# Performance work log

Measured on AMD Instinct MI355X. Metric: run time of the kernel, lower is better.

Reference implementation:

```python
import jax, jax.numpy as jnp
import numpy as np

N_NODES = 20000
N_EDGES = 160000
CIN = 2000
N1 = 500
N2 = 250
DIM_Z = 16


def _xavier(key, shape):
    fan_out, fan_in = shape
    lim = jnp.sqrt(6.0 / (fan_in + fan_out))
    return jax.random.uniform(key, shape, jnp.float32, -lim, lim)


def setup_inputs() -> dict:
    key = jax.random.key(0)
    ks = jax.random.split(key, 10)
    data_in = jax.random.normal(ks[0], (N_NODES, CIN), jnp.float32)
    edge_index = jax.random.randint(ks[1], (2, N_EDGES), 0, N_NODES, jnp.int64)
    edge_weight = jax.random.uniform(ks[2], (N_EDGES,), jnp.float32)
    return {
        "data_in": data_in,
        "edge_index": edge_index,
        "edge_weight": edge_weight,
        "W1": _xavier(ks[3], (N1, CIN)),
        "b1": jnp.zeros((N1,), jnp.float32),
        "W2": _xavier(ks[4], (N2, N1)),
        "b2": jnp.zeros((N2,), jnp.float32),
        "W_mu_t": _xavier(ks[5], (1, N2)),
        "b_mu_t": jnp.zeros((1,), jnp.float32),
        "W_std_t": _xavier(ks[6], (1, N2)),
        "b_std_t": jnp.zeros((1,), jnp.float32),
        "W_mu_z": _xavier(ks[7], (DIM_Z, N2)),
        "b_mu_z": jnp.zeros((DIM_Z,), jnp.float32),
        "W_std_z": _xavier(ks[8], (DIM_Z, N2)),
        "b_std_z": jnp.zeros((DIM_Z,), jnp.float32),
    }


def gcn_conv(x, W, b, src, dst, ew, n_nodes):
    """PyG GCNConv: add self-loops (weight 1), symmetric deg^-1/2 normalization,
    linear transform, scatter-add aggregate to target nodes, add bias."""
    loop = jnp.arange(n_nodes, dtype=src.dtype)
    src_f = jnp.concatenate([src, loop])
    dst_f = jnp.concatenate([dst, loop])
    ew_f = jnp.concatenate([ew, jnp.ones((n_nodes,), ew.dtype)])
    deg = jax.ops.segment_sum(ew_f, dst_f, num_segments=n_nodes)
    dinv = jnp.where(deg > 0, jax.lax.rsqrt(deg), 0.0)
    norm = dinv[src_f] * ew_f * dinv[dst_f]  # [E+N]
    h = x @ W.T                               # [N, F_out]
    msgs = h[src_f] * norm[:, None]           # [E+N, F_out] gathered messages
    out = jax.ops.segment_sum(msgs, dst_f, num_segments=n_nodes)
    return out + b


def reference(data_in, edge_index, edge_weight, W1, b1, W2, b2,
              W_mu_t, b_mu_t, W_std_t, b_std_t, W_mu_z, b_mu_z, W_std_z, b_std_z):
    src, dst = edge_index[0], edge_index[1]
    n = data_in.shape[0]
    h = gcn_conv(data_in, W1, b1, src, dst, edge_weight, n)
    h = gcn_conv(h, W2, b2, src, dst, edge_weight, n)
    mu_tx = jax.nn.softplus(h @ W_mu_t.T + b_mu_t)
    std_tx = jax.nn.softplus(h @ W_std_t.T + b_std_t)
    mu_zx = h @ W_mu_z.T + b_mu_z
    std_zx = jax.nn.softplus(h @ W_std_z.T + b_std_z)
    return (mu_tx, std_tx, mu_zx, std_zx)
```

## Files before the change

kernel.cpp:

```cpp
#include <hip/hip_runtime.h>

#define N_NODES 20000
#define N_EDGES 160000
#define CIN     2000
#define N1      500
#define N2      250
#define NH      34
#define NHP     64

typedef __attribute__((ext_vector_type(4))) float f32x4;
typedef __attribute__((ext_vector_type(8))) __bf16 bf16x8;
typedef __attribute__((ext_vector_type(8))) unsigned short ushort8;

typedef const __attribute__((address_space(1))) void* as1cv;
typedef __attribute__((address_space(3))) void* as3v;

__device__ __forceinline__ unsigned short f2bf(float f) {
    unsigned int u = __builtin_bit_cast(unsigned int, f);
    u += 0x7FFFu + ((u >> 16) & 1u);
    return (unsigned short)(u >> 16);
}

__device__ __forceinline__ ushort8 pack8(float4 a, float4 b) {
    ushort8 r;
    r[0] = f2bf(a.x); r[1] = f2bf(a.y); r[2] = f2bf(a.z); r[3] = f2bf(a.w);
    r[4] = f2bf(b.x); r[5] = f2bf(b.y); r[6] = f2bf(b.z); r[7] = f2bf(b.w);
    return r;
}

__global__ __launch_bounds__(256) void k1(
    const int* __restrict__ ei, const float* __restrict__ ew,
    float* degsum, int* cnt,
    const float* __restrict__ W2,
    const float* __restrict__ Wmt, const float* __restrict__ Wst,
    const float* __restrict__ Wmz, const float* __restrict__ Wsz,
    float* __restrict__ V, unsigned short* __restrict__ Vb,
    const float* __restrict__ W1, unsigned short* __restrict__ W1T) {
    __shared__ float tile[32][33];
    const int B = blockIdx.x, t = threadIdx.x;
    if (B < 625) {
        int e = B * 256 + t;
        if (e < N_EDGES) {
            int d = ei[N_EDGES + e];
            atomicAdd(&degsum[d], ew[e]);
            atomicAdd(&cnt[d], 1);
        }
        return;
    }
    if (B < 753) {
        float* wh = &tile[0][0];
        int b = B - 625;
        int o = b >> 1, half = b & 1;
        int n = half * 256 + t;
        if (o >= NH) {
            V[(size_t)o * 512 + n] = 0.f;
            Vb[(size_t)o * 512 + n] = 0;
            return;
        }
        const float* src; int row;
        if (o == 0)      { src = Wmt; row = 0; }
        else if (o == 1) { src = Wst; row = 0; }
        else if (o < 18) { src = Wmz; row = o - 2; }
        else             { src = Wsz; row = o - 18; }
        if (t < N2) wh[t] = src[(size_t)row * N2 + t];
        __syncthreads();
        float acc = 0.f;
        if (n < N1) {
            for (int j = 0; j < N2; ++j) acc += wh[j] * W2[(size_t)j * N1 + n];
        }
        float v = (n < N1) ? acc : 0.f;
        V[(size_t)o * 512 + n] = v;
        Vb[(size_t)o * 512 + n] = f2bf(v);
        return;
    }
    int bb = B - 753;
    int jt = bb & 15, nt = bb >> 4;
    int c = t & 31, r = t >> 5;
#pragma unroll
    for (int i = 0; i < 4; ++i) {
        int j = jt * 32 + r + i * 8;
        int n = nt * 32 + c;
        tile[r + i * 8][c] = (j < N1 && n < CIN) ? W1[(size_t)j * CIN + n] : 0.f;
    }
    __syncthreads();
#pragma unroll
    for (int i = 0; i < 4; ++i) {
        int n = nt * 32 + r + i * 8;
        int j = jt * 32 + c;
        W1T[(size_t)n * 512 + j] = f2bf(tile[c][r + i * 8]);
    }
}

__global__ __launch_bounds__(256) void k2(
    const int* __restrict__ cnt, const float* __restrict__ degsum,
    float* __restrict__ dinv, int* __restrict__ rowPtr, int* __restrict__ cursor,
    const unsigned short* __restrict__ Vb, const unsigned short* __restrict__ W1T,
    unsigned short* __restrict__ Wtb,
    const float* __restrict__ V,
    const float* __restrict__ b1, const float* __restrict__ b2,
    const float* __restrict__ bmt, const float* __restrict__ bst,
    const float* __restrict__ bmz, const float* __restrict__ bsz,
    const float* __restrict__ Wmt, const float* __restrict__ Wst,
    const float* __restrict__ Wmz, const float* __restrict__ Wsz,
    float* __restrict__ ccdd) {
    __shared__ alignas(16) unsigned short lA[128 * 32];
    __shared__ alignas(16) unsigned short lB[128 * 32];
    __shared__ int sdata[256];
    const int B = blockIdx.x, t = threadIdx.x;
    if (B < 79) {
        const int nbase = B * 256;
        int idx = nbase + t;
        if (idx < N_NODES) cursor[idx] = 0;
        int s = 0;
        for (int i = t; i < nbase; i += 256) s += cnt[i];
        sdata[t] = s;
        __syncthreads();
        for (int off = 128; off; off >>= 1) {
            if (t < off) sdata[t] += sdata[t + off];
            __syncthreads();
        }
        const int base = sdata[0];
        __syncthreads();
        int v = 0;
        if (idx < N_NODES) {
            v = cnt[idx];
            dinv[idx] = rsqrtf(1.0f + degsum[idx]);
        }
        sdata[t] = v;
        __syncthreads();
        for (int off = 1; off < 256; off <<= 1) {
            int x = (t >= off) ? sdata[t - off] : 0;
            __syncthreads();
            sdata[t] += x;
            __syncthreads();
        }
        if (idx < N_NODES) rowPtr[idx] = base + sdata[t] - v;
        if (B == 78 && t == 255) rowPtr[N_NODES] = base + sdata[255];
        return;
    }
    if (B == 79) {
        int w = t >> 6, lane = t & 63;
        for (int o = w; o < NH; o += 4) {
            float cc = 0.f;
            for (int n = lane; n < N1; n += 64) cc += V[(size_t)o * 512 + n] * b1[n];
            const float* src; int row; float bias;
            if (o == 0)      { src = Wmt; row = 0;      bias = bmt[0]; }
            else if (o == 1) { src = Wst; row = 0;      bias = bst[0]; }
            else if (o < 18) { src = Wmz; row = o - 2;  bias = bmz[o - 2]; }
            else             { src = Wsz; row = o - 18; bias = bsz[o - 18]; }
            float dd = 0.f;
            for (int j = lane; j < N2; j += 64) dd += src[(size_t)row * N2 + j] * b2[j];
#pragma unroll
            for (int off = 32; off; off >>= 1) {
                cc += __shfl_down(cc, off);
                dd += __shfl_down(dd, off);
            }
            if (lane == 0) { ccdd[o] = cc; ccdd[NHP + o] = dd + bias; }
        }
        if (t >= NH && t < NHP) { ccdd[t] = 0.f; ccdd[NHP + t] = 0.f; }
        return;
    }
    {
        const int w = t >> 6, lane = t & 63;
        const int bn0 = (B - 80) * 128;
        const int M = 64;
        const int wr = w >> 1, wc = w & 1;
        const int lr = lane & 15, lk = (lane >> 4) * 8;
        f32x4 acc[4][4];
#pragma unroll
        for (int i = 0; i < 4; i++)
#pragma unroll
            for (int j = 0; j < 4; j++) acc[i][j] = (f32x4){0.f, 0.f, 0.f, 0.f};
        for (int kt = 0; kt < 16; ++kt) {
            const int kb = kt * 32;
#pragma unroll
            for (int i = 0; i < 2; i++) {
                int c0 = i * 256 + w * 64;
                int c  = c0 + lane;
                int rr = c >> 2, kg = c & 3;
                int grow = rr < M ? rr : M - 1;
                const unsigned short* gp = Vb + (size_t)grow * 512 + kb + kg * 8;
                __builtin_amdgcn_global_load_lds((as1cv)gp, (as3v)(lA + (size_t)c0 * 8), 16, 0, 0);
            }
#pragma unroll
            for (int i = 0; i < 2; i++) {
                int c0 = i * 256 + w * 64;
                int c  = c0 + lane;
                int rr = c >> 2, kg = c & 3;
                const unsigned short* gp = W1T + (size_t)(bn0 + rr) * 512 + kb + kg * 8;
                __builtin_amdgcn_global_load_lds((as1cv)gp, (as3v)(lB + (size_t)c0 * 8), 16, 0, 0);
            }
            __syncthreads();
            ushort8 af[4], bfr[4];
#pragma unroll
            for (int m = 0; m < 4; m++)
                af[m] = *reinterpret_cast<const ushort8*>(&lA[(wr * 64 + m * 16 + lr) * 32 + lk]);
#pragma unroll
            for (int n = 0; n < 4; n++)
                bfr[n] = *reinterpret_cast<const ushort8*>(&lB[(wc * 64 + n * 16 + lr) * 32 + lk]);
#pragma unroll
            for (int m = 0; m < 4; m++)
#pragma unroll
                for (int n = 0; n < 4; n++)
                    acc[m][n] = __builtin_amdgcn_mfma_f32_16x16x32_bf16(
                        __builtin_bit_cast(bf16x8, af[m]), __builtin_bit_cast(bf16x8, bfr[n]),
                        acc[m][n], 0, 0, 0);
            __syncthreads();
        }
        const int crow0 = wr * 64 + (lane >> 4) * 4;
        const int ccol0 = bn0 + wc * 64 + lr;
#pragma unroll
        for (int m = 0; m < 4; m++)
#pragma unroll
            for (int n = 0; n < 4; n++)
#pragma unroll
                for (int rg = 0; rg < 4; rg++) {
                    int row = crow0 + m * 16 + rg;
                    if (row < M)
                        Wtb[(size_t)row * 2048 + ccol0 + n * 16] = f2bf(acc[m][n][rg]);
                }
    }
}

__global__ __launch_bounds__(256) void k3(
    const float* __restrict__ X, const unsigned short* __restrict__ Wtb,
    float* __restrict__ Tpart,
    const int* __restrict__ ei, const float* __restrict__ ew,
    const float* __restrict__ dinv, const int* __restrict__ rowPtr,
    int* cursor, int* __restrict__ colA, float* __restrict__ valA) {
    __shared__ alignas(16) unsigned short lA[64 * 64];
    __shared__ alignas(16) unsigned short lB[64 * 64];
    const int B = blockIdx.x, t = threadIdx.x;
    if (B >= 626) {
        int e = (B - 626) * 256 + t;
        if (e < N_EDGES) {
            int s = ei[e], d = ei[N_EDGES + e];
            int p = atomicAdd(&cursor[d], 1);
            int j = rowPtr[d] + p;
            colA[j] = s;
            valA[j] = dinv[s] * ew[e] * dinv[d];
        }
        return;
    }
    const int w = t >> 6, lane = t & 63;
    const int kp = B & 1;
    const int bm0 = (B >> 1) * 64;
    const int kbase = kp * 1024;
    const int lr = lane & 15, lkb = (lane >> 4) * 16;

    const int c0 = t, c1 = t + 256;
    const int ar0 = c0 >> 3, ac0 = (c0 & 7) * 8;
    const int ar1 = c1 >> 3, ac1 = (c1 & 7) * 8;
    int gr0 = bm0 + ar0; if (gr0 >= N_NODES) gr0 = N_NODES - 1;
    int gr1 = bm0 + ar1; if (gr1 >= N_NODES) gr1 = N_NODES - 1;
    const float* pA0 = X + (size_t)gr0 * CIN + kbase + ac0;
    const float* pA1 = X + (size_t)gr1 * CIN + kbase + ac1;
    const unsigned short* pB0 = Wtb + ar0 * 2048 + kbase + ac0;
    const unsigned short* pB1 = Wtb + ar1 * 2048 + kbase + ac1;
    char* const LA = (char*)lA;
    char* const LB = (char*)lB;
    char* const wA0 = LA + ((ar0 * 128 + ac0 * 2) ^ ((ar0 & 7) << 4));
    char* const wA1 = LA + ((ar1 * 128 + ac1 * 2) ^ ((ar1 & 7) << 4));
    char* const wB0 = LB + ((ar0 * 128 + ac0 * 2) ^ ((ar0 & 7) << 4));
    char* const wB1 = LB + ((ar1 * 128 + ac1 * 2) ^ ((ar1 & 7) << 4));

    int aoff[4][2], boff[2];
#pragma unroll
    for (int m = 0; m < 4; ++m)
#pragma unroll
        for (int k = 0; k < 2; ++k)
            aoff[m][k] = (((m * 16 + lr) * 128 + k * 64 + lkb) ^ ((lr & 7) << 4));
#pragma unroll
    for (int k = 0; k < 2; ++k)
        boff[k] = (((w * 16 + lr) * 128 + k * 64 + lkb) ^ ((lr & 7) << 4));

    f32x4 acc[4];
#pragma unroll
    for (int m = 0; m < 4; ++m) acc[m] = (f32x4){0.f, 0.f, 0.f, 0.f};

    float4 a00A, a01A, a10A, a11A; ushort8 bv0A, bv1A;
    float4 a00B, a01B, a10B, a11B; ushort8 bv0B, bv1B;
    const float4 z4 = make_float4(0.f, 0.f, 0.f, 0.f);

#define STAGE_LOAD(S, a00_, a01_, a10_, a11_, bv0_, bv1_)                          \
    {                                                                              \
        bool v0 = (kbase + ac0 + (S) * 64) < CIN;                                  \
        bool v1 = (kbase + ac1 + (S) * 64) < CIN;                                  \
        const float4* q0 = (const float4*)(v0 ? pA0 + (S) * 64 : (const float*)X); \
        const float4* q1 = (const float4*)(v1 ? pA1 + (S) * 64 : (const float*)X); \
        a00_ = q0[0]; a01_ = q0[1];                                                \
        a10_ = q1[0]; a11_ = q1[1];                                                \
        if (!v0) { a00_ = z4; a01_ = z4; }                                         \
        if (!v1) { a10_ = z4; a11_ = z4; }                                         \
        bv0_ = *(const ushort8*)(pB0 + (S) * 64);                                  \
        bv1_ = *(const ushort8*)(pB1 + (S) * 64);                                  \
    }

    auto compute = [&]() {
#pragma unroll
        for (int k = 0; k < 2; ++k) {
            ushort8 bf = *(const ushort8*)(LB + boff[k]);
#pragma unroll
            for (int m = 0; m < 4; ++m) {
                ushort8 af = *(const ushort8*)(LA + aoff[m][k]);
                acc[m] = __builtin_amdgcn_mfma_f32_16x16x32_bf16(
                    __builtin_bit_cast(bf16x8, af), __builtin_bit_cast(bf16x8, bf),
                    acc[m], 0, 0, 0);
            }
        }
    };

    STAGE_LOAD(0, a00A, a01A, a10A, a11A, bv0A, bv1A)
    STAGE_LOAD(1, a00B, a01B, a10B, a11B, bv0B, bv1B)
    for (int s2 = 0; s2 < 8; ++s2) {
        const int s = 2 * s2;
        __syncthreads();
        *(ushort8*)wA0 = pack8(a00A, a01A);
        *(ushort8*)wA1 = pack8(a10A, a11A);
        *(ushort8*)wB0 = bv0A;
        *(ushort8*)wB1 = bv1A;
        __syncthreads();
        if (s + 2 < 16) STAGE_LOAD(s + 2, a00A, a01A, a10A, a11A, bv0A, bv1A)
        compute();
        __syncthreads();
        *(ushort8*)wA0 = pack8(a00B, a01B);
        *(ushort8*)wA1 = pack8(a10B, a11B);
        *(ushort8*)wB0 = bv0B;
        *(ushort8*)wB1 = bv1B;
        __syncthreads();
        if (s + 3 < 16) STAGE_LOAD(s + 3, a00B, a01B, a10B, a11B, bv0B, bv1B)
        compute();
    }
#undef STAGE_LOAD
    float* Tp = Tpart + (size_t)kp * N_NODES * NHP;
    const int col = w * 16 + lr;
    const int rb = bm0 + (lane >> 4) * 4;
#pragma unroll
    for (int m = 0; m < 4; ++m)
#pragma unroll
        for (int rg = 0; rg < 4; ++rg) {
            int row = rb + m * 16 + rg;
            if (row < N_NODES) Tp[(size_t)row * NHP + col] = acc[m][rg];
        }
}

__global__ __launch_bounds__(256) void agg_a(
    const float* __restrict__ Tp, const int* __restrict__ rowPtr,
    const int* __restrict__ colA, const float* __restrict__ valA,
    const float* __restrict__ dinv, float* __restrict__ U) {
    const float* __restrict__ T1 = Tp + (size_t)N_NODES * NHP;
    int wid = blockIdx.x * 4 + (threadIdx.x >> 6);
    int lane = threadIdx.x & 63;
    if (wid >= N_NODES) return;
    int d = wid;
    float dv = dinv[d];
    float acc = dv * dv * (Tp[(size_t)d * NHP + lane] + T1[(size_t)d * NHP + lane]);
    int e0 = rowPtr[d], e1 = rowPtr[d + 1];
    int e = e0;
    for (; e + 8 <= e1; e += 8) {
        int   s0 = colA[e],     s1 = colA[e + 1], s2 = colA[e + 2], s3 = colA[e + 3];
        int   s4 = colA[e + 4], s5 = colA[e + 5], s6 = colA[e + 6], s7 = colA[e + 7];
        float w0 = valA[e],     w1 = valA[e + 1], w2 = valA[e + 2], w3 = valA[e + 3];
        float w4 = valA[e + 4], w5 = valA[e + 5], w6 = valA[e + 6], w7 = valA[e + 7];
        float t0 = Tp[(size_t)s0 * NHP + lane] + T1[(size_t)s0 * NHP + lane];
        float t1 = Tp[(size_t)s1 * NHP + lane] + T1[(size_t)s1 * NHP + lane];
        float t2 = Tp[(size_t)s2 * NHP + lane] + T1[(size_t)s2 * NHP + lane];
        float t3 = Tp[(size_t)s3 * NHP + lane] + T1[(size_t)s3 * NHP + lane];
        float t4 = Tp[(size_t)s4 * NHP + lane] + T1[(size_t)s4 * NHP + lane];
        float t5 = Tp[(size_t)s5 * NHP + lane] + T1[(size_t)s5 * NHP + lane];
        float t6 = Tp[(size_t)s6 * NHP + lane] + T1[(size_t)s6 * NHP + lane];
        float t7 = Tp[(size_t)s7 * NHP + lane] + T1[(size_t)s7 * NHP + lane];
        acc += w0 * t0 + w1 * t1 + w2 * t2 + w3 * t3
             + w4 * t4 + w5 * t5 + w6 * t6 + w7 * t7;
    }
    for (; e + 4 <= e1; e += 4) {
        int s0 = colA[e], s1 = colA[e + 1], s2 = colA[e + 2], s3 = colA[e + 3];
        float w0 = valA[e], w1 = valA[e + 1], w2 = valA[e + 2], w3 = valA[e + 3];
        float t0 = Tp[(size_t)s0 * NHP + lane] + T1[(size_t)s0 * NHP + lane];
        float t1 = Tp[(size_t)s1 * NHP + lane] + T1[(size_t)s1 * NHP + lane];
        float t2 = Tp[(size_t)s2 * NHP + lane] + T1[(size_t)s2 * NHP + lane];
        float t3 = Tp[(size_t)s3 * NHP + lane] + T1[(size_t)s3 * NHP + lane];
        acc += w0 * t0 + w1 * t1 + w2 * t2 + w3 * t3;
    }
    for (; e < e1; ++e) {
        int s = colA[e];
        acc += valA[e] * (Tp[(size_t)s * NHP + lane] + T1[(size_t)s * NHP + lane]);
    }
    U[(size_t)d * NHP + lane] = acc;
}

__global__ __launch_bounds__(256) void agg_b(
    const float* __restrict__ U, const int* __restrict__ rowPtr,
    const int* __restrict__ colA, const float* __restrict__ valA,
    const float* __restrict__ dinv, const float* __restrict__ ccdd,
    float* __restrict__ out) {
    int wid = blockIdx.x * 4 + (threadIdx.x >> 6);
    int lane = threadIdx.x & 63;
    if (wid >= N_NODES) return;
    int d = wid;
    float dv = dinv[d], self = dv * dv;
    float acc = self * U[(size_t)d * NHP + lane];
    float r = self;
    int e0 = rowPtr[d], e1 = rowPtr[d + 1];
    int e = e0;
    for (; e + 8 <= e1; e += 8) {
        int   s0 = colA[e],     s1 = colA[e + 1], s2 = colA[e + 2], s3 = colA[e + 3];
        int   s4 = colA[e + 4], s5 = colA[e + 5], s6 = colA[e + 6], s7 = colA[e + 7];
        float w0 = valA[e],     w1 = valA[e + 1], w2 = valA[e + 2], w3 = valA[e + 3];
        float w4 = valA[e + 4], w5 = valA[e + 5], w6 = valA[e + 6], w7 = valA[e + 7];
        float t0 = U[(size_t)s0 * NHP + lane], t1 = U[(size_t)s1 * NHP + lane];
        float t2 = U[(size_t)s2 * NHP + lane], t3 = U[(size_t)s3 * NHP + lane];
        float t4 = U[(size_t)s4 * NHP + lane], t5 = U[(size_t)s5 * NHP + lane];
        float t6 = U[(size_t)s6 * NHP + lane], t7 = U[(size_t)s7 * NHP + lane];
        acc += w0 * t0 + w1 * t1 + w2 * t2 + w3 * t3
             + w4 * t4 + w5 * t5 + w6 * t6 + w7 * t7;
        r += w0 + w1 + w2 + w3 + w4 + w5 + w6 + w7;
    }
    for (; e + 4 <= e1; e += 4) {
        int s0 = colA[e], s1 = colA[e + 1], s2 = colA[e + 2], s3 = colA[e + 3];
        float w0 = valA[e], w1 = valA[e + 1], w2 = valA[e + 2], w3 = valA[e + 3];
        float t0 = U[(size_t)s0 * NHP + lane], t1 = U[(size_t)s1 * NHP + lane];
        float t2 = U[(size_t)s2 * NHP + lane], t3 = U[(size_t)s3 * NHP + lane];
        acc += w0 * t0 + w1 * t1 + w2 * t2 + w3 * t3;
        r += w0 + w1 + w2 + w3;
    }
    for (; e < e1; ++e) {
        int s = colA[e];
        float wv = valA[e];
        acc += wv * U[(size_t)s * NHP + lane];
        r += wv;
    }
    if (lane < NH) {
        float v = acc + r * ccdd[lane] + ccdd[NHP + lane];
        if (lane < 2 || lane >= 18)
            v = fmaxf(v, 0.f) + log1pf(expf(-fabsf(v)));
        size_t oidx;
        if (lane == 0)      oidx = (size_t)d;
        else if (lane == 1) oidx = (size_t)N_NODES + d;
        else if (lane < 18) oidx = (size_t)2 * N_NODES + (size_t)d * 16 + (lane - 2);
        else                oidx = (size_t)18 * N_NODES + (size_t)d * 16 + (lane - 18);
        out[oidx] = v;
    }
}

extern "C" void kernel_launch(void* const* d_in, const int* in_sizes, int n_in,
                              void* d_out, int out_size, void* d_ws, size_t ws_size,
                              hipStream_t stream) {
    const float* X   = (const float*)d_in[0];
    const int*   EI  = (const int*)d_in[1];
    const float* EW  = (const float*)d_in[2];
    const float* W1  = (const float*)d_in[3];
    const float* b1  = (const float*)d_in[4];
    const float* W2  = (const float*)d_in[5];
    const float* b2  = (const float*)d_in[6];
    const float* Wmt = (const float*)d_in[7];
    const float* bmt = (const float*)d_in[8];
    const float* Wst = (const float*)d_in[9];
    const float* bst = (const float*)d_in[10];
    const float* Wmz = (const float*)d_in[11];
    const float* bmz = (const float*)d_in[12];
    const float* Wsz = (const float*)d_in[13];
    const float* bsz = (const float*)d_in[14];
    float* out = (float*)d_out;

    char* ws = (char*)d_ws;
    size_t off = 0;
    auto alloc = [&](size_t bytes) -> char* {
        char* p = ws + off;
        off += (bytes + 255) & ~(size_t)255;
        return p;
    };
    float*          V    = (float*)alloc((size_t)NHP * 512 * 4);
    unsigned short* Vb   = (unsigned short*)alloc((size_t)NHP * 512 * 2);
    unsigned short* W1T  = (unsigned short*)alloc((size_t)2048 * 512 * 2);
    unsigned short* Wtb  = (unsigned short*)alloc((size_t)NHP * 2048 * 2);
    float*          ccdd = (float*)alloc(2 * NHP * 4);
    float*          Tp   = (float*)alloc((size_t)2 * N_NODES * NHP * 4);
    float*          U    = (float*)alloc((size_t)N_NODES * NHP * 4);
    float* degsum = (float*)alloc(N_NODES * 4);
    int*   cnt    = (int*)alloc(N_NODES * 4);
    int*   cursor = (int*)alloc(N_NODES * 4);
    float* dinv   = (float*)alloc(N_NODES * 4);
    int*   rowPtr = (int*)alloc((N_NODES + 1) * 4);
    int*   colA   = (int*)alloc(N_EDGES * 4);
    float* valA   = (float*)alloc(N_EDGES * 4);
    if (off > ws_size) return;

    size_t zspan = (size_t)((char*)(cnt + N_NODES) - (char*)degsum);
    hipMemsetAsync(degsum, 0, zspan, stream);

    k1<<<625 + 128 + 1024, 256, 0, stream>>>(EI, EW, degsum, cnt,
                                             W2, Wmt, Wst, Wmz, Wsz, V, Vb, W1, W1T);
    k2<<<79 + 1 + 16, 256, 0, stream>>>(cnt, degsum, dinv, rowPtr, cursor,
                                        Vb, W1T, Wtb, V,
                                        b1, b2, bmt, bst, bmz, bsz, Wmt, Wst, Wmz, Wsz, ccdd);
    k3<<<626 + 625, 256, 0, stream>>>(X, Wtb, Tp, EI, EW, dinv, rowPtr, cursor, colA, valA);
    agg_a<<<(N_NODES + 3) / 4, 256, 0, stream>>>(Tp, rowPtr, colA, valA, dinv, U);
    agg_b<<<(N_NODES + 3) / 4, 256, 0, stream>>>(U, rowPtr, colA, valA, dinv, ccdd, out);
}
```

Baseline: 123.5 us.

## Fuse GEMM, CSR fill and both aggregations into persistent kernel with grid barriers

Merges k3, agg_a and agg_b into one persistent kernel of 512 blocks that loops over the former work units and separates the phases with a two-level software tree barrier built on agent-scope atomics. Intermediate stores use relaxed agent-scope atomic stores so later phases can see them. This removes two kernel launches and their gaps, at the cost of fewer resident blocks for the GEMM phase and reliance on all 512 blocks being co-resident. The k1 W2 reduction loop is also unrolled by 8.

```diff
diff --git a/kernel.cpp b/kernel.cpp
--- a/kernel.cpp
+++ b/kernel.cpp
@@ -7,6 +7,7 @@
 #define N2      250
 #define NH      34
 #define NHP     64
+#define MEGA_BLK 512
 
 typedef __attribute__((ext_vector_type(4))) float f32x4;
 typedef __attribute__((ext_vector_type(8))) __bf16 bf16x8;
@@ -26,6 +27,40 @@
     r[0] = f2bf(a.x); r[1] = f2bf(a.y); r[2] = f2bf(a.z); r[3] = f2bf(a.w);
     r[4] = f2bf(b.x); r[5] = f2bf(b.y); r[6] = f2bf(b.z); r[7] = f2bf(b.w);
     return r;
+}
+
+__device__ __forceinline__ void ast(float* p, float v) {
+    __hip_atomic_store(p, v, __ATOMIC_RELAXED, __HIP_MEMORY_SCOPE_AGENT);
+}
+__device__ __forceinline__ void asti(int* p, int v) {
+    __hip_atomic_store(p, v, __ATOMIC_RELAXED, __HIP_MEMORY_SCOPE_AGENT);
+}
+
+__device__ __forceinline__ void tree_barrier(int* bars) {
+    asm volatile("s_waitcnt vmcnt(0)" ::: "memory");
+    __syncthreads();
+    if (threadIdx.x == 0) {
+        int g = blockIdx.x & 15;
+        int* gcnt = bars + g * 32;
+        int* ggen = bars + g * 32 + 16;
+        int* rcnt = bars + 512;
+        int* rgen = bars + 528;
+        int a = __hip_atomic_fetch_add(gcnt, 1, __ATOMIC_RELAXED, __HIP_MEMORY_SCOPE_AGENT);
+        if (a == 31) {
+            int r = __hip_atomic_fetch_add(rcnt, 1, __ATOMIC_RELAXED, __HIP_MEMORY_SCOPE_AGENT);
+            if (r == 15) {
+                __hip_atomic_store(rgen, 1, __ATOMIC_RELAXED, __HIP_MEMORY_SCOPE_AGENT);
+            } else {
+                while (__hip_atomic_load(rgen, __ATOMIC_RELAXED, __HIP_MEMORY_SCOPE_AGENT) == 0)
+                    __builtin_amdgcn_s_sleep(16);
+            }
+            __hip_atomic_store(ggen, 1, __ATOMIC_RELAXED, __HIP_MEMORY_SCOPE_AGENT);
+        } else {
+            while (__hip_atomic_load(ggen, __ATOMIC_RELAXED, __HIP_MEMORY_SCOPE_AGENT) == 0)
+                __builtin_amdgcn_s_sleep(16);
+        }
+    }
+    __syncthreads();
 }
 
 __global__ __launch_bounds__(256) void k1(
@@ -66,7 +101,17 @@
         __syncthreads();
         float acc = 0.f;
         if (n < N1) {
-            for (int j = 0; j < N2; ++j) acc += wh[j] * W2[(size_t)j * N1 + n];
+            const float* p = W2 + n;
+            int j = 0;
+            for (; j + 8 <= N2; j += 8) {
+                float x0 = p[(size_t)(j + 0) * N1], x1 = p[(size_t)(j + 1) * N1];
+                float x2 = p[(size_t)(j + 2) * N1], x3 = p[(size_t)(j + 3) * N1];
+                float x4 = p[(size_t)(j + 4) * N1], x5 = p[(size_t)(j + 5) * N1];
+                float x6 = p[(size_t)(j + 6) * N1], x7 = p[(size_t)(j + 7) * N1];
+                acc += wh[j] * x0 + wh[j + 1] * x1 + wh[j + 2] * x2 + wh[j + 3] * x3
+                     + wh[j + 4] * x4 + wh[j + 5] * x5 + wh[j + 6] * x6 + wh[j + 7] * x7;
+            }
+            for (; j < N2; ++j) acc += wh[j] * p[(size_t)j * N1];
         }
         float v = (n < N1) ? acc : 0.f;
         V[(size_t)o * 512 + n] = v;
@@ -102,7 +147,7 @@
     const float* __restrict__ bmz, const float* __restrict__ bsz,
     const float* __restrict__ Wmt, const float* __restrict__ Wst,
     const float* __restrict__ Wmz, const float* __restrict__ Wsz,
-    float* __restrict__ ccdd) {
+    float* __restrict__ ccdd, int* __restrict__ bars) {
     __shared__ alignas(16) unsigned short lA[128 * 32];
     __shared__ alignas(16) unsigned short lB[128 * 32];
     __shared__ int sdata[256];
@@ -139,6 +184,7 @@
         return;
     }
     if (B == 79) {
+        for (int i = t; i < 1088; i += 256) bars[i] = 0;
         int w = t >> 6, lane = t & 63;
         for (int o = w; o < NH; o += 4) {
             float cc = 0.f;
@@ -222,65 +268,70 @@
     }
 }
 
-__global__ __launch_bounds__(256) void k3(
+__global__ __launch_bounds__(256, 2) void k3mega(
     const float* __restrict__ X, const unsigned short* __restrict__ Wtb,
-    float* __restrict__ Tpart,
+    float* __restrict__ Tp,
     const int* __restrict__ ei, const float* __restrict__ ew,
     const float* __restrict__ dinv, const int* __restrict__ rowPtr,
-    int* cursor, int* __restrict__ colA, float* __restrict__ valA) {
+    int* cursor, int* __restrict__ colA, float* __restrict__ valA,
+    float* __restrict__ U, const float* __restrict__ ccdd,
+    float* __restrict__ out, int* __restrict__ bars) {
     __shared__ alignas(16) unsigned short lA[64 * 64];
     __shared__ alignas(16) unsigned short lB[64 * 64];
     const int B = blockIdx.x, t = threadIdx.x;
-    if (B >= 626) {
-        int e = (B - 626) * 256 + t;
-        if (e < N_EDGES) {
-            int s = ei[e], d = ei[N_EDGES + e];
-            int p = atomicAdd(&cursor[d], 1);
-            int j = rowPtr[d] + p;
-            colA[j] = s;
-            valA[j] = dinv[s] * ew[e] * dinv[d];
-        }
-        return;
-    }
-    const int w = t >> 6, lane = t & 63;
-    const int kp = B & 1;
-    const int bm0 = (B >> 1) * 64;
-    const int kbase = kp * 1024;
-    const int lr = lane & 15, lkb = (lane >> 4) * 16;
-
-    const int c0 = t, c1 = t + 256;
-    const int ar0 = c0 >> 3, ac0 = (c0 & 7) * 8;
-    const int ar1 = c1 >> 3, ac1 = (c1 & 7) * 8;
-    int gr0 = bm0 + ar0; if (gr0 >= N_NODES) gr0 = N_NODES - 1;
-    int gr1 = bm0 + ar1; if (gr1 >= N_NODES) gr1 = N_NODES - 1;
-    const float* pA0 = X + (size_t)gr0 * CIN + kbase + ac0;
-    const float* pA1 = X + (size_t)gr1 * CIN + kbase + ac1;
-    const unsigned short* pB0 = Wtb + ar0 * 2048 + kbase + ac0;
-    const unsigned short* pB1 = Wtb + ar1 * 2048 + kbase + ac1;
-    char* const LA = (char*)lA;
-    char* const LB = (char*)lB;
-    char* const wA0 = LA + ((ar0 * 128 + ac0 * 2) ^ ((ar0 & 7) << 4));
-    char* const wA1 = LA + ((ar1 * 128 + ac1 * 2) ^ ((ar1 & 7) << 4));
-    char* const wB0 = LB + ((ar0 * 128 + ac0 * 2) ^ ((ar0 & 7) << 4));
-    char* const wB1 = LB + ((ar1 * 128 + ac1 * 2) ^ ((ar1 & 7) << 4));
-
-    int aoff[4][2], boff[2];
-#pragma unroll
-    for (int m = 0; m < 4; ++m)
+    const int lane = t & 63;
+
+    for (int u = B; u < 1251; u += MEGA_BLK) {
+        if (u >= 626) {
+            int e = (u - 626) * 256 + t;
+            if (e < N_EDGES) {
+                int s = ei[e], d = ei[N_EDGES + e];
+                int p = atomicAdd(&cursor[d], 1);
+                int j = rowPtr[d] + p;
+                asti(&colA[j], s);
+                ast(&valA[j], dinv[s] * ew[e] * dinv[d]);
+            }
+            continue;
+        }
+        const int w = t >> 6;
+        const int kp = u & 1;
+        const int bm0 = (u >> 1) * 64;
+        const int kbase = kp * 1024;
+        const int lr = lane & 15, lkb = (lane >> 4) * 16;
+
+        const int c0 = t, c1 = t + 256;
+        const int ar0 = c0 >> 3, ac0 = (c0 & 7) * 8;
+        const int ar1 = c1 >> 3, ac1 = (c1 & 7) * 8;
+        int gr0 = bm0 + ar0; if (gr0 >= N_NODES) gr0 = N_NODES - 1;
+        int gr1 = bm0 + ar1; if (gr1 >= N_NODES) gr1 = N_NODES - 1;
+        const float* pA0 = X + (size_t)gr0 * CIN + kbase + ac0;
+        const float* pA1 = X + (size_t)gr1 * CIN + kbase + ac1;
+        const unsigned short* pB0 = Wtb + ar0 * 2048 + kbase + ac0;
+        const unsigned short* pB1 = Wtb + ar1 * 2048 + kbase + ac1;
+        char* const LA = (char*)lA;
+        char* const LB = (char*)lB;
+        char* const wA0 = LA + ((ar0 * 128 + ac0 * 2) ^ ((ar0 & 7) << 4));
+        char* const wA1 = LA + ((ar1 * 128 + ac1 * 2) ^ ((ar1 & 7) << 4));
+        char* const wB0 = LB + ((ar0 * 128 + ac0 * 2) ^ ((ar0 & 7) << 4));
+        char* const wB1 = LB + ((ar1 * 128 + ac1 * 2) ^ ((ar1 & 7) << 4));
+
+        int aoff[4][2], boff[2];
+#pragma unroll
+        for (int m = 0; m < 4; ++m)
+#pragma unroll
+            for (int k = 0; k < 2; ++k)
+                aoff[m][k] = (((m * 16 + lr) * 128 + k * 64 + lkb) ^ ((lr & 7) << 4));
 #pragma unroll
         for (int k = 0; k < 2; ++k)
-            aoff[m][k] = (((m * 16 + lr) * 128 + k * 64 + lkb) ^ ((lr & 7) << 4));
-#pragma unroll
-    for (int k = 0; k < 2; ++k)
-        boff[k] = (((w * 16 + lr) * 128 + k * 64 + lkb) ^ ((lr & 7) << 4));
-
-    f32x4 acc[4];
-#pragma unroll
-    for (int m = 0; m < 4; ++m) acc[m] = (f32x4){0.f, 0.f, 0.f, 0.f};
-
-    float4 a00A, a01A, a10A, a11A; ushort8 bv0A, bv1A;
-    float4 a00B, a01B, a10B, a11B; ushort8 bv0B, bv1B;
-    const float4 z4 = make_float4(0.f, 0.f, 0.f, 0.f);
+            boff[k] = (((w * 16 + lr) * 128 + k * 64 + lkb) ^ ((lr & 7) << 4));
+
+        f32x4 acc[4];
+#pragma unroll
+        for (int m = 0; m < 4; ++m) acc[m] = (f32x4){0.f, 0.f, 0.f, 0.f};
+
+        float4 a00A, a01A, a10A, a11A; ushort8 bv0A, bv1A;
+        float4 a00B, a01B, a10B, a11B; ushort8 bv0B, bv1B;
+        const float4 z4 = make_float4(0.f, 0.f, 0.f, 0.f);
 
 #define STAGE_LOAD(S, a00_, a01_, a10_, a11_, bv0_, bv1_)                          \
     {                                                                              \
@@ -296,150 +347,128 @@
         bv1_ = *(const ushort8*)(pB1 + (S) * 64);                                  \
     }
 
-    auto compute = [&]() {
-#pragma unroll
-        for (int k = 0; k < 2; ++k) {
-            ushort8 bf = *(const ushort8*)(LB + boff[k]);
-#pragma unroll
-            for (int m = 0; m < 4; ++m) {
-                ushort8 af = *(const ushort8*)(LA + aoff[m][k]);
-                acc[m] = __builtin_amdgcn_mfma_f32_16x16x32_bf16(
-                    __builtin_bit_cast(bf16x8, af), __builtin_bit_cast(bf16x8, bf),
-                    acc[m], 0, 0, 0);
-            }
-        }
-    };
-
-    STAGE_LOAD(0, a00A, a01A, a10A, a11A, bv0A, bv1A)
-    STAGE_LOAD(1, a00B, a01B, a10B, a11B, bv0B, bv1B)
-    for (int s2 = 0; s2 < 8; ++s2) {
-        const int s = 2 * s2;
-        __syncthreads();
-        *(ushort8*)wA0 = pack8(a00A, a01A);
-        *(ushort8*)wA1 = pack8(a10A, a11A);
-        *(ushort8*)wB0 = bv0A;
-        *(ushort8*)wB1 = bv1A;
-        __syncthreads();
-        if (s + 2 < 16) STAGE_LOAD(s + 2, a00A, a01A, a10A, a11A, bv0A, bv1A)
-        compute();
-        __syncthreads();
-        *(ushort8*)wA0 = pack8(a00B, a01B);
-        *(ushort8*)wA1 = pack8(a10B, a11B);
-        *(ushort8*)wB0 = bv0B;
-        *(ushort8*)wB1 = bv1B;
-        __syncthreads();
-        if (s + 3 < 16) STAGE_LOAD(s + 3, a00B, a01B, a10B, a11B, bv0B, bv1B)
-        compute();
-    }
+        auto compute = [&]() {
+#pragma unroll
+            for (int k = 0; k < 2; ++k) {
+                ushort8 bf = *(const ushort8*)(LB + boff[k]);
+#pragma unroll
+                for (int m = 0; m < 4; ++m) {
+                    ushort8 af = *(const ushort8*)(LA + aoff[m][k]);
+                    acc[m] = __builtin_amdgcn_mfma_f32_16x16x32_bf16(
+                        __builtin_bit_cast(bf16x8, af), __builtin_bit_cast(bf16x8, bf),
+                        acc[m], 0, 0, 0);
+                }
+            }
+        };
+
+        STAGE_LOAD(0, a00A, a01A, a10A, a11A, bv0A, bv1A)
+        STAGE_LOAD(1, a00B, a01B, a10B, a11B, bv0B, bv1B)
+        for (int s2 = 0; s2 < 8; ++s2) {
+            const int s = 2 * s2;
+            __syncthreads();
+            *(ushort8*)wA0 = pack8(a00A, a01A);
+            *(ushort8*)wA1 = pack8(a10A, a11A);
+            *(ushort8*)wB0 = bv0A;
+            *(ushort8*)wB1 = bv1A;
+            __syncthreads();
+            if (s + 2 < 16) STAGE_LOAD(s + 2, a00A, a01A, a10A, a11A, bv0A, bv1A)
+            compute();
+            __syncthreads();
+            *(ushort8*)wA0 = pack8(a00B, a01B);
+            *(ushort8*)wA1 = pack8(a10B, a11B);
+            *(ushort8*)wB0 = bv0B;
+            *(ushort8*)wB1 = bv1B;
+            __syncthreads();
+            if (s + 3 < 16) STAGE_LOAD(s + 3, a00B, a01B, a10B, a11B, bv0B, bv1B)
+            compute();
+        }
 #undef STAGE_LOAD
-    float* Tp = Tpart + (size_t)kp * N_NODES * NHP;
-    const int col = w * 16 + lr;
-    const int rb = bm0 + (lane >> 4) * 4;
-#pragma unroll
-    for (int m = 0; m < 4; ++m)
-#pragma unroll
-        for (int rg = 0; rg < 4; ++rg) {
-            int row = rb + m * 16 + rg;
-            if (row < N_NODES) Tp[(size_t)row * NHP + col] = acc[m][rg];
-        }
-}
-
-__global__ __launch_bounds__(256) void agg_a(
-    const float* __restrict__ Tp, const int* __restrict__ rowPtr,
-    const int* __restrict__ colA, const float* __restrict__ valA,
-    const float* __restrict__ dinv, float* __restrict__ U) {
-    const float* __restrict__ T1 = Tp + (size_t)N_NODES * NHP;
-    int wid = blockIdx.x * 4 + (threadIdx.x >> 6);
-    int lane = threadIdx.x & 63;
-    if (wid >= N_NODES) return;
-    int d = wid;
-    float dv = dinv[d];
-    float acc = dv * dv * (Tp[(size_t)d * NHP + lane] + T1[(size_t)d * NHP + lane]);
-    int e0 = rowPtr[d], e1 = rowPtr[d + 1];
-    int e = e0;
-    for (; e + 8 <= e1; e += 8) {
-        int   s0 = colA[e],     s1 = colA[e + 1], s2 = colA[e + 2], s3 = colA[e + 3];
-        int   s4 = colA[e + 4], s5 = colA[e + 5], s6 = colA[e + 6], s7 = colA[e + 7];
-        float w0 = valA[e],     w1 = valA[e + 1], w2 = valA[e + 2], w3 = valA[e + 3];
-        float w4 = valA[e + 4], w5 = valA[e + 5], w6 = valA[e + 6], w7 = valA[e + 7];
-        float t0 = Tp[(size_t)s0 * NHP + lane] + T1[(size_t)s0 * NHP + lane];
-        float t1 = Tp[(size_t)s1 * NHP + lane] + T1[(size_t)s1 * NHP + lane];
-        float t2 = Tp[(size_t)s2 * NHP + lane] + T1[(size_t)s2 * NHP + lane];
-        float t3 = Tp[(size_t)s3 * NHP + lane] + T1[(size_t)s3 * NHP + lane];
-        float t4 = Tp[(size_t)s4 * NHP + lane] + T1[(size_t)s4 * NHP + lane];
-        float t5 = Tp[(size_t)s5 * NHP + lane] + T1[(size_t)s5 * NHP + lane];
-        float t6 = Tp[(size_t)s6 * NHP + lane] + T1[(size_t)s6 * NHP + lane];
-        float t7 = Tp[(size_t)s7 * NHP + lane] + T1[(size_t)s7 * NHP + lane];
-        acc += w0 * t0 + w1 * t1 + w2 * t2 + w3 * t3
-             + w4 * t4 + w5 * t5 + w6 * t6 + w7 * t7;
-    }
-    for (; e + 4 <= e1; e += 4) {
-        int s0 = colA[e], s1 = colA[e + 1], s2 = colA[e + 2], s3 = colA[e + 3];
-        float w0 = valA[e], w1 = valA[e + 1], w2 = valA[e + 2], w3 = valA[e + 3];
-        float t0 = Tp[(size_t)s0 * NHP + lane] + T1[(size_t)s0 * NHP + lane];
-        float t1 = Tp[(size_t)s1 * NHP + lane] + T1[(size_t)s1 * NHP + lane];
-        float t2 = Tp[(size_t)s2 * NHP + lane] + T1[(size_t)s2 * NHP + lane];
-        float t3 = Tp[(size_t)s3 * NHP + lane] + T1[(size_t)s3 * NHP + lane];
-        acc += w0 * t0 + w1 * t1 + w2 * t2 + w3 * t3;
-    }
-    for (; e < e1; ++e) {
-        int s = colA[e];
-        acc += valA[e] * (Tp[(size_t)s * NHP + lane] + T1[(size_t)s * NHP + lane]);
-    }
-    U[(size_t)d * NHP + lane] = acc;
-}
-
-__global__ __launch_bounds__(256) void agg_b(
-    const float* __restrict__ U, const int* __restrict__ rowPtr,
-    const int* __restrict__ colA, const float* __restrict__ valA,
-    const float* __restrict__ dinv, const float* __restrict__ ccdd,
-    float* __restrict__ out) {
-    int wid = blockIdx.x * 4 + (threadIdx.x >> 6);
-    int lane = threadIdx.x & 63;
-    if (wid >= N_NODES) return;
-    int d = wid;
-    float dv = dinv[d], self = dv * dv;
-    float acc = self * U[(size_t)d * NHP + lane];
-    float r = self;
-    int e0 = rowPtr[d], e1 = rowPtr[d + 1];
-    int e = e0;
-    for (; e + 8 <= e1; e += 8) {
-        int   s0 = colA[e],     s1 = colA[e + 1], s2 = colA[e + 2], s3 = colA[e + 3];
-        int   s4 = colA[e + 4], s5 = colA[e + 5], s6 = colA[e + 6], s7 = colA[e + 7];
-        float w0 = valA[e],     w1 = valA[e + 1], w2 = valA[e + 2], w3 = valA[e + 3];
-        float w4 = valA[e + 4], w5 = valA[e + 5], w6 = valA[e + 6], w7 = valA[e + 7];
-        float t0 = U[(size_t)s0 * NHP + lane], t1 = U[(size_t)s1 * NHP + lane];
-        float t2 = U[(size_t)s2 * NHP + lane], t3 = U[(size_t)s3 * NHP + lane];
-        float t4 = U[(size_t)s4 * NHP + lane], t5 = U[(size_t)s5 * NHP + lane];
-        float t6 = U[(size_t)s6 * NHP + lane], t7 = U[(size_t)s7 * NHP + lane];
-        acc += w0 * t0 + w1 * t1 + w2 * t2 + w3 * t3
-             + w4 * t4 + w5 * t5 + w6 * t6 + w7 * t7;
-        r += w0 + w1 + w2 + w3 + w4 + w5 + w6 + w7;
-    }
-    for (; e + 4 <= e1; e += 4) {
-        int s0 = colA[e], s1 = colA[e + 1], s2 = colA[e + 2], s3 = colA[e + 3];
-        float w0 = valA[e], w1 = valA[e + 1], w2 = valA[e + 2], w3 = valA[e + 3];
-        float t0 = U[(size_t)s0 * NHP + lane], t1 = U[(size_t)s1 * NHP + lane];
-        float t2 = U[(size_t)s2 * NHP + lane], t3 = U[(size_t)s3 * NHP + lane];
-        acc += w0 * t0 + w1 * t1 + w2 * t2 + w3 * t3;
-        r += w0 + w1 + w2 + w3;
-    }
-    for (; e < e1; ++e) {
-        int s = colA[e];
-        float wv = valA[e];
-        acc += wv * U[(size_t)s * NHP + lane];
-        r += wv;
-    }
-    if (lane < NH) {
-        float v = acc + r * ccdd[lane] + ccdd[NHP + lane];
-        if (lane < 2 || lane >= 18)
-            v = fmaxf(v, 0.f) + log1pf(expf(-fabsf(v)));
-        size_t oidx;
-        if (lane == 0)      oidx = (size_t)d;
-        else if (lane == 1) oidx = (size_t)N_NODES + d;
-        else if (lane < 18) oidx = (size_t)2 * N_NODES + (size_t)d * 16 + (lane - 2);
-        else                oidx = (size_t)18 * N_NODES + (size_t)d * 16 + (lane - 18);
-        out[oidx] = v;
+        float* TpK = Tp + (size_t)kp * N_NODES * NHP;
+        const int col = w * 16 + lr;
+        const int rb = bm0 + (lane >> 4) * 4;
+#pragma unroll
+        for (int m = 0; m < 4; ++m)
+#pragma unroll
+            for (int rg = 0; rg < 4; ++rg) {
+                int row = rb + m * 16 + rg;
+                if (row < N_NODES) ast(&TpK[(size_t)row * NHP + col], acc[m][rg]);
+            }
+    }
+
+    tree_barrier(bars);
+
+    {
+        const float* __restrict__ T0 = Tp;
+        const float* __restrict__ T1 = Tp + (size_t)N_NODES * NHP;
+        for (int uu = B; uu < N_NODES / 4; uu += MEGA_BLK) {
+            int d = uu * 4 + (t >> 6);
+            float dv = dinv[d];
+            float acc = dv * dv * (T0[(size_t)d * NHP + lane] + T1[(size_t)d * NHP + lane]);
+            int e0 = rowPtr[d], e1 = rowPtr[d + 1];
+            int e = e0;
+            for (; e + 8 <= e1; e += 8) {
+                int   s0 = colA[e],     s1 = colA[e + 1], s2 = colA[e + 2], s3 = colA[e + 3];
+                int   s4 = colA[e + 4], s5 = colA[e + 5], s6 = colA[e + 6], s7 = colA[e + 7];
+                float w0 = valA[e],     w1 = valA[e + 1], w2 = valA[e + 2], w3 = valA[e + 3];
+                float w4 = valA[e + 4], w5 = valA[e + 5], w6 = valA[e + 6], w7 = valA[e + 7];
+                float t0 = T0[(size_t)s0 * NHP + lane] + T1[(size_t)s0 * NHP + lane];
+                float t1 = T0[(size_t)s1 * NHP + lane] + T1[(size_t)s1 * NHP + lane];
+                float t2 = T0[(size_t)s2 * NHP + lane] + T1[(size_t)s2 * NHP + lane];
+                float t3 = T0[(size_t)s3 * NHP + lane] + T1[(size_t)s3 * NHP + lane];
+                float t4 = T0[(size_t)s4 * NHP + lane] + T1[(size_t)s4 * NHP + lane];
+                float t5 = T0[(size_t)s5 * NHP + lane] + T1[(size_t)s5 * NHP + lane];
+                float t6 = T0[(size_t)s6 * NHP + lane] + T1[(size_t)s6 * NHP + lane];
+                float t7 = T0[(size_t)s7 * NHP + lane] + T1[(size_t)s7 * NHP + lane];
+                acc += w0 * t0 + w1 * t1 + w2 * t2 + w3 * t3
+                     + w4 * t4 + w5 * t5 + w6 * t6 + w7 * t7;
+            }
+            for (; e < e1; ++e) {
+                int s = colA[e];
+                acc += valA[e] * (T0[(size_t)s * NHP + lane] + T1[(size_t)s * NHP + lane]);
+            }
+            ast(&U[(size_t)d * NHP + lane], acc);
+        }
+    }
+
+    tree_barrier(bars + 544);
+
+    for (int uu = B; uu < N_NODES / 4; uu += MEGA_BLK) {
+        int d = uu * 4 + (t >> 6);
+        float dv = dinv[d], self = dv * dv;
+        float acc = self * U[(size_t)d * NHP + lane];
+        float r = self;
+        int e0 = rowPtr[d], e1 = rowPtr[d + 1];
+        int e = e0;
+        for (; e + 8 <= e1; e += 8) {
+            int   s0 = colA[e],     s1 = colA[e + 1], s2 = colA[e + 2], s3 = colA[e + 3];
+            int   s4 = colA[e + 4], s5 = colA[e + 5], s6 = colA[e + 6], s7 = colA[e + 7];
+            float w0 = valA[e],     w1 = valA[e + 1], w2 = valA[e + 2], w3 = valA[e + 3];
+            float w4 = valA[e + 4], w5 = valA[e + 5], w6 = valA[e + 6], w7 = valA[e + 7];
+            float t0 = U[(size_t)s0 * NHP + lane], t1 = U[(size_t)s1 * NHP + lane];
+            float t2 = U[(size_t)s2 * NHP + lane], t3 = U[(size_t)s3 * NHP + lane];
+            float t4 = U[(size_t)s4 * NHP + lane], t5 = U[(size_t)s5 * NHP + lane];
+            float t6 = U[(size_t)s6 * NHP + lane], t7 = U[(size_t)s7 * NHP + lane];
+            acc += w0 * t0 + w1 * t1 + w2 * t2 + w3 * t3
+                 + w4 * t4 + w5 * t5 + w6 * t6 + w7 * t7;
+            r += w0 + w1 + w2 + w3 + w4 + w5 + w6 + w7;
+        }
+        for (; e < e1; ++e) {
+            int s = colA[e];
+            float wv = valA[e];
+            acc += wv * U[(size_t)s * NHP + lane];
+            r += wv;
+        }
+        if (lane < NH) {
+            float v = acc + r * ccdd[lane] + ccdd[NHP + lane];
+            if (lane < 2 || lane >= 18)
+                v = fmaxf(v, 0.f) + log1pf(expf(-fabsf(v)));
+            size_t oidx;
+            if (lane == 0)      oidx = (size_t)d;
+            else if (lane == 1) oidx = (size_t)N_NODES + d;
+            else if (lane < 18) oidx = (size_t)2 * N_NODES + (size_t)d * 16 + (lane - 2);
+            else                oidx = (size_t)18 * N_NODES + (size_t)d * 16 + (lane - 18);
+            out[oidx] = v;
+        }
     }
 }
 
@@ -484,6 +513,7 @@
     int*   rowPtr = (int*)alloc((N_NODES + 1) * 4);
     int*   colA   = (int*)alloc(N_EDGES * 4);
     float* valA   = (float*)alloc(N_EDGES * 4);
+    int*   bars   = (int*)alloc(1088 * 4);
     if (off > ws_size) return;
 
     size_t zspan = (size_t)((char*)(cnt + N_NODES) - (char*)degsum);
@@ -493,8 +523,8 @@
                                              W2, Wmt, Wst, Wmz, Wsz, V, Vb, W1, W1T);
     k2<<<79 + 1 + 16, 256, 0, stream>>>(cnt, degsum, dinv, rowPtr, cursor,
                                         Vb, W1T, Wtb, V,
-                                        b1, b2, bmt, bst, bmz, bsz, Wmt, Wst, Wmz, Wsz, ccdd);
-    k3<<<626 + 625, 256, 0, stream>>>(X, Wtb, Tp, EI, EW, dinv, rowPtr, cursor, colA, valA);
-    agg_a<<<(N_NODES + 3) / 4, 256, 0, stream>>>(Tp, rowPtr, colA, valA, dinv, U);
-    agg_b<<<(N_NODES + 3) / 4, 256, 0, stream>>>(U, rowPtr, colA, valA, dinv, ccdd, out);
-}
+                                        b1, b2, bmt, bst, bmz, bsz, Wmt, Wst, Wmz, Wsz,
+                                        ccdd, bars);
+    k3mega<<<MEGA_BLK, 256, 0, stream>>>(X, Wtb, Tp, EI, EW, dinv, rowPtr,
+                                         cursor, colA, valA, U, ccdd, out, bars);
+}
```

Result: slower. 173.4 us (+40.5%).

## Store aggregation intermediates in bf16 and pre-reduce split-K partials

Applied to the files above, without the earlier changes.

Adds a reduce_T kernel that sums the two split-K partial outputs and stores them as bf16. Both aggregation passes then gather bf16 rows instead of two or one fp32 rows, which cuts the bytes fetched per edge gather by a factor of two to four. The intermediate U is also kept in bf16. The W2-fold loop in k1 is unrolled by eight to expose more independent loads. The cost is an extra kernel launch, one extra pass over Tp, and reduced precision in the intermediates.

```diff
diff --git a/kernel.cpp b/kernel.cpp
--- a/kernel.cpp
+++ b/kernel.cpp
@@ -11,6 +11,7 @@
 typedef __attribute__((ext_vector_type(4))) float f32x4;
 typedef __attribute__((ext_vector_type(8))) __bf16 bf16x8;
 typedef __attribute__((ext_vector_type(8))) unsigned short ushort8;
+typedef __attribute__((ext_vector_type(4))) unsigned short us4;
 
 typedef const __attribute__((address_space(1))) void* as1cv;
 typedef __attribute__((address_space(3))) void* as3v;
@@ -19,6 +20,10 @@
     unsigned int u = __builtin_bit_cast(unsigned int, f);
     u += 0x7FFFu + ((u >> 16) & 1u);
     return (unsigned short)(u >> 16);
+}
+__device__ __forceinline__ float bf2f(unsigned short h) {
+    unsigned int u = ((unsigned int)h) << 16;
+    return __builtin_bit_cast(float, u);
 }
 
 __device__ __forceinline__ ushort8 pack8(float4 a, float4 b) {
@@ -66,7 +71,17 @@
         __syncthreads();
         float acc = 0.f;
         if (n < N1) {
-            for (int j = 0; j < N2; ++j) acc += wh[j] * W2[(size_t)j * N1 + n];
+            const float* p = W2 + n;
+            int j = 0;
+            for (; j + 8 <= N2; j += 8) {
+                float x0 = p[(size_t)(j + 0) * N1], x1 = p[(size_t)(j + 1) * N1];
+                float x2 = p[(size_t)(j + 2) * N1], x3 = p[(size_t)(j + 3) * N1];
+                float x4 = p[(size_t)(j + 4) * N1], x5 = p[(size_t)(j + 5) * N1];
+                float x6 = p[(size_t)(j + 6) * N1], x7 = p[(size_t)(j + 7) * N1];
+                acc += wh[j] * x0 + wh[j + 1] * x1 + wh[j + 2] * x2 + wh[j + 3] * x3
+                     + wh[j + 4] * x4 + wh[j + 5] * x5 + wh[j + 6] * x6 + wh[j + 7] * x7;
+            }
+            for (; j < N2; ++j) acc += wh[j] * p[(size_t)j * N1];
         }
         float v = (n < N1) ? acc : 0.f;
         V[(size_t)o * 512 + n] = v;
@@ -344,17 +359,30 @@
         }
 }
 
+__global__ __launch_bounds__(256) void reduce_T(
+    const float* __restrict__ Tp, unsigned short* __restrict__ T16) {
+    const int n4 = N_NODES * NHP / 4;
+    int i = blockIdx.x * 256 + threadIdx.x;
+    if (i < n4) {
+        float4 a = reinterpret_cast<const float4*>(Tp)[i];
+        float4 b = reinterpret_cast<const float4*>(Tp + (size_t)N_NODES * NHP)[i];
+        us4 o;
+        o[0] = f2bf(a.x + b.x); o[1] = f2bf(a.y + b.y);
+        o[2] = f2bf(a.z + b.z); o[3] = f2bf(a.w + b.w);
+        reinterpret_cast<us4*>(T16)[i] = o;
+    }
+}
+
 __global__ __launch_bounds__(256) void agg_a(
-    const float* __restrict__ Tp, const int* __restrict__ rowPtr,
+    const unsigned short* __restrict__ T16, const int* __restrict__ rowPtr,
     const int* __restrict__ colA, const float* __restrict__ valA,
-    const float* __restrict__ dinv, float* __restrict__ U) {
-    const float* __restrict__ T1 = Tp + (size_t)N_NODES * NHP;
+    const float* __restrict__ dinv, unsigned short* __restrict__ U16) {
     int wid = blockIdx.x * 4 + (threadIdx.x >> 6);
     int lane = threadIdx.x & 63;
     if (wid >= N_NODES) return;
     int d = wid;
     float dv = dinv[d];
-    float acc = dv * dv * (Tp[(size_t)d * NHP + lane] + T1[(size_t)d * NHP + lane]);
+    float acc = dv * dv * bf2f(T16[(size_t)d * NHP + lane]);
     int e0 = rowPtr[d], e1 = rowPtr[d + 1];
     int e = e0;
     for (; e + 8 <= e1; e += 8) {
@@ -362,35 +390,22 @@
         int   s4 = colA[e + 4], s5 = colA[e + 5], s6 = colA[e + 6], s7 = colA[e + 7];
         float w0 = valA[e],     w1 = valA[e + 1], w2 = valA[e + 2], w3 = valA[e + 3];
         float w4 = valA[e + 4], w5 = valA[e + 5], w6 = valA[e + 6], w7 = valA[e + 7];
-        float t0 = Tp[(size_t)s0 * NHP + lane] + T1[(size_t)s0 * NHP + lane];
-        float t1 = Tp[(size_t)s1 * NHP + lane] + T1[(size_t)s1 * NHP + lane];
-        float t2 = Tp[(size_t)s2 * NHP + lane] + T1[(size_t)s2 * NHP + lane];
-        float t3 = Tp[(size_t)s3 * NHP + lane] + T1[(size_t)s3 * NHP + lane];
-        float t4 = Tp[(size_t)s4 * NHP + lane] + T1[(size_t)s4 * NHP + lane];
-        float t5 = Tp[(size_t)s5 * NHP + lane] + T1[(size_t)s5 * NHP + lane];
-        float t6 = Tp[(size_t)s6 * NHP + lane] + T1[(size_t)s6 * NHP + lane];
-        float t7 = Tp[(size_t)s7 * NHP + lane] + T1[(size_t)s7 * NHP + lane];
+        float t0 = bf2f(T16[(size_t)s0 * NHP + lane]), t1 = bf2f(T16[(size_t)s1 * NHP + lane]);
+        float t2 = bf2f(T16[(size_t)s2 * NHP + lane]), t3 = bf2f(T16[(size_t)s3 * NHP + lane]);
+        float t4 = bf2f(T16[(size_t)s4 * NHP + lane]), t5 = bf2f(T16[(size_t)s5 * NHP + lane]);
+        float t6 = bf2f(T16[(size_t)s6 * NHP + lane]), t7 = bf2f(T16[(size_t)s7 * NHP + lane]);
         acc += w0 * t0 + w1 * t1 + w2 * t2 + w3 * t3
              + w4 * t4 + w5 * t5 + w6 * t6 + w7 * t7;
     }
-    for (; e + 4 <= e1; e += 4) {
-        int s0 = colA[e], s1 = colA[e + 1], s2 = colA[e + 2], s3 = colA[e + 3];
-        float w0 = valA[e], w1 = valA[e + 1], w2 = valA[e + 2], w3 = valA[e + 3];
-        float t0 = Tp[(size_t)s0 * NHP + lane] + T1[(size_t)s0 * NHP + lane];
-        float t1 = Tp[(size_t)s1 * NHP + lane] + T1[(size_t)s1 * NHP + lane];
-        float t2 = Tp[(size_t)s2 * NHP + lane] + T1[(size_t)s2 * NHP + lane];
-        float t3 = Tp[(size_t)s3 * NHP + lane] + T1[(size_t)s3 * NHP + lane];
-        acc += w0 * t0 + w1 * t1 + w2 * t2 + w3 * t3;
-    }
     for (; e < e1; ++e) {
         int s = colA[e];
-        acc += valA[e] * (Tp[(size_t)s * NHP + lane] + T1[(size_t)s * NHP + lane]);
-    }
-    U[(size_t)d * NHP + lane] = acc;
+        acc += valA[e] * bf2f(T16[(size_t)s * NHP + lane]);
+    }
+    U16[(size_t)d * NHP + lane] = f2bf(acc);
 }
 
 __global__ __launch_bounds__(256) void agg_b(
-    const float* __restrict__ U, const int* __restrict__ rowPtr,
+    const unsigned short* __restrict__ U16, const int* __restrict__ rowPtr,
     const int* __restrict__ colA, const float* __restrict__ valA,
     const float* __restrict__ dinv, const float* __restrict__ ccdd,
     float* __restrict__ out) {
@@ -399,7 +414,7 @@
     if (wid >= N_NODES) return;
     int d = wid;
     float dv = dinv[d], self = dv * dv;
-    float acc = self * U[(size_t)d * NHP + lane];
+    float acc = self * bf2f(U16[(size_t)d * NHP + lane]);
     float r = self;
     int e0 = rowPtr[d], e1 = rowPtr[d + 1];
     int e = e0;
@@ -408,26 +423,18 @@
         int   s4 = colA[e + 4], s5 = colA[e + 5], s6 = colA[e + 6], s7 = colA[e + 7];
         float w0 = valA[e],     w1 = valA[e + 1], w2 = valA[e + 2], w3 = valA[e + 3];
         float w4 = valA[e + 4], w5 = valA[e + 5], w6 = valA[e + 6], w7 = valA[e + 7];
-        float t0 = U[(size_t)s0 * NHP + lane], t1 = U[(size_t)s1 * NHP + lane];
-        float t2 = U[(size_t)s2 * NHP + lane], t3 = U[(size_t)s3 * NHP + lane];
-        float t4 = U[(size_t)s4 * NHP + lane], t5 = U[(size_t)s5 * NHP + lane];
-        float t6 = U[(size_t)s6 * NHP + lane], t7 = U[(size_t)s7 * NHP + lane];
+        float t0 = bf2f(U16[(size_t)s0 * NHP + lane]), t1 = bf2f(U16[(size_t)s1 * NHP + lane]);
+        float t2 = bf2f(U16[(size_t)s2 * NHP + lane]), t3 = bf2f(U16[(size_t)s3 * NHP + lane]);
+        float t4 = bf2f(U16[(size_t)s4 * NHP + lane]), t5 = bf2f(U16[(size_t)s5 * NHP + lane]);
+        float t6 = bf2f(U16[(size_t)s6 * NHP + lane]), t7 = bf2f(U16[(size_t)s7 * NHP + lane]);
         acc += w0 * t0 + w1 * t1 + w2 * t2 + w3 * t3
              + w4 * t4 + w5 * t5 + w6 * t6 + w7 * t7;
         r += w0 + w1 + w2 + w3 + w4 + w5 + w6 + w7;
     }
-    for (; e + 4 <= e1; e += 4) {
-        int s0 = colA[e], s1 = colA[e + 1], s2 = colA[e + 2], s3 = colA[e + 3];
-        float w0 = valA[e], w1 = valA[e + 1], w2 = valA[e + 2], w3 = valA[e + 3];
-        float t0 = U[(size_t)s0 * NHP + lane], t1 = U[(size_t)s1 * NHP + lane];
-        float t2 = U[(size_t)s2 * NHP + lane], t3 = U[(size_t)s3 * NHP + lane];
-        acc += w0 * t0 + w1 * t1 + w2 * t2 + w3 * t3;
-        r += w0 + w1 + w2 + w3;
-    }
     for (; e < e1; ++e) {
         int s = colA[e];
         float wv = valA[e];
-        acc += wv * U[(size_t)s * NHP + lane];
+        acc += wv * bf2f(U16[(size_t)s * NHP + lane]);
         r += wv;
     }
     if (lane < NH) {
@@ -476,7 +483,8 @@
     unsigned short* Wtb  = (unsigned short*)alloc((size_t)NHP * 2048 * 2);
     float*          ccdd = (float*)alloc(2 * NHP * 4);
     float*          Tp   = (float*)alloc((size_t)2 * N_NODES * NHP * 4);
-    float*          U    = (float*)alloc((size_t)N_NODES * NHP * 4);
+    unsigned short* T16  = (unsigned short*)alloc((size_t)N_NODES * NHP * 2);
+    unsigned short* U16  = (unsigned short*)alloc((size_t)N_NODES * NHP * 2);
     float* degsum = (float*)alloc(N_NODES * 4);
     int*   cnt    = (int*)alloc(N_NODES * 4);
     int*   cursor = (int*)alloc(N_NODES * 4);
@@ -487,7 +495,7 @@
     if (off > ws_size) return;
 
     size_t zspan = (size_t)((char*)(cnt + N_NODES) - (char*)degsum);
-    hipMemsetAsync(degsum, 0, zspan, stream);
+    (void)hipMemsetAsync(degsum, 0, zspan, stream);
 
     k1<<<625 + 128 + 1024, 256, 0, stream>>>(EI, EW, degsum, cnt,
                                              W2, Wmt, Wst, Wmz, Wsz, V, Vb, W1, W1T);
@@ -495,6 +503,7 @@
                                         Vb, W1T, Wtb, V,
                                         b1, b2, bmt, bst, bmz, bsz, Wmt, Wst, Wmz, Wsz, ccdd);
     k3<<<626 + 625, 256, 0, stream>>>(X, Wtb, Tp, EI, EW, dinv, rowPtr, cursor, colA, valA);
-    agg_a<<<(N_NODES + 3) / 4, 256, 0, stream>>>(Tp, rowPtr, colA, valA, dinv, U);
-    agg_b<<<(N_NODES + 3) / 4, 256, 0, stream>>>(U, rowPtr, colA, valA, dinv, ccdd, out);
-}
+    reduce_T<<<(N_NODES * NHP / 4 + 255) / 256, 256, 0, stream>>>(Tp, T16);
+    agg_a<<<(N_NODES + 3) / 4, 256, 0, stream>>>(T16, rowPtr, colA, valA, dinv, U16);
+    agg_b<<<(N_NODES + 3) / 4, 256, 0, stream>>>(U16, rowPtr, colA, valA, dinv, ccdd, out);
+}
```

Result: slower. 129.1 us (+4.6%).
